# Optimization experiments

Measured on AMD Instinct MI355X. Metric: run time of the kernel, lower is better.

Reference implementation:

```python
import jax, jax.numpy as jnp
import numpy as np

B, N, F_IN = 4, 2048, 256
K, D = 4, 64
NEG_SLOPE = 0.2


def setup_inputs() -> dict:
    key = jax.random.key(0)
    k1, k2, k3, k4, k5 = jax.random.split(key, 5)
    x = jax.random.normal(k1, (B, N, F_IN), dtype=jnp.float32)
    adj = jax.random.randint(k2, (B, N, N), 0, 2, dtype=jnp.int32)
    # xavier_uniform-style params
    def xavier(k, shape):
        fan_in, fan_out = shape[-2], shape[-1]
        lim = np.sqrt(6.0 / (fan_in + fan_out))
        return jax.random.uniform(k, shape, jnp.float32, -lim, lim)
    W = xavier(k3, (K, F_IN, D))
    a_src = xavier(k4, (K, D, 1))
    a_dst = xavier(k5, (K, D, 1))
    return {"x": x, "adj": adj, "W": W, "a_src": a_src, "a_dst": a_dst}


def reference(x, adj, W, a_src, a_dst):
    # Wh: (B, K, N, D)
    Wh = jnp.einsum('bnf,kfd->bknd', x, W)
    e_src = jnp.einsum('bknd,kdo->bkno', Wh, a_src)  # (B,K,N,1)
    e_dst = jnp.einsum('bknd,kdo->bkno', Wh, a_dst)  # (B,K,N,1)
    e = e_src + jnp.swapaxes(e_dst, -2, -1)          # (B,K,N,N)
    e = jnp.where(e > 0, e, NEG_SLOPE * e)           # LeakyReLU(0.2)
    # adjacency mask with forced self-loops (adj + I > 0)
    eye = jnp.eye(e.shape[-1], dtype=bool)
    mask = (adj[:, None, :, :] > 0) | eye            # (B,1|K,N,N)
    e = jnp.where(mask, e, -jnp.inf)
    # numerically-stable softmax matching F_module_softmax
    x_max = jnp.max(e, axis=-1, keepdims=True)
    x_max = jnp.where(jnp.isinf(x_max), 0.0, x_max)
    exp_e = jnp.exp(e - x_max)
    exp_e = jnp.where(jnp.isinf(e), 0.0, exp_e)
    alpha = exp_e / (jnp.sum(exp_e, axis=-1, keepdims=True) + 1e-10)
    # dropout is identity in eval mode
    out = jnp.matmul(alpha, Wh)                      # (B,K,N,D)
    # concat heads: (B,N,K*D)
    Bn, Kn, Nn, Dn = out.shape
    return jnp.transpose(out, (0, 2, 1, 3)).reshape(Bn, Nn, Kn * Dn)
```

## Files before the change

### kernel.cpp

```cpp
#include <hip/hip_runtime.h>

#define NB 4
#define NN 2048
#define NF 256
#define NK 4
#define ND 64
#define NEG 0.2f
#define LOG2E 1.4426950408889634f

typedef _Float16 f16;
typedef _Float16 f16x2 __attribute__((ext_vector_type(2)));
typedef _Float16 f16x4 __attribute__((ext_vector_type(4)));
typedef _Float16 f16x8 __attribute__((ext_vector_type(8)));
typedef float f32x4 __attribute__((ext_vector_type(4)));
typedef float f32x16 __attribute__((ext_vector_type(16)));
typedef unsigned int u32;
typedef unsigned short u16;

__global__ __launch_bounds__(256) void k01(
    const float* __restrict__ x,
    const int*   __restrict__ adj,
    const float* __restrict__ Wm,
    const float* __restrict__ a_src,
    const float* __restrict__ a_dst,
    unsigned int* __restrict__ abit,
    f16* __restrict__ wht,
    float* __restrict__ sbuf,
    f16* __restrict__ ebuf,
    f16* __restrict__ fbuf)
{
    __shared__ f16 wt[64 * 256];

    const int bx  = blockIdx.x;
    const int tid = threadIdx.x;

    if (bx >= 256) {
        const int row = (bx - 256) * 4 + (tid >> 6);
        const int l   = tid & 63;
        const int i   = row & (NN - 1);
        const int* __restrict__ ar = adj + (size_t)row * NN;

        int v[32];
#pragma unroll
        for (int c = 0; c < 32; ++c) v[c] = ar[c * 64 + l];

        unsigned int kx = 0, ky = 0;
#pragma unroll
        for (int c = 0; c < 32; ++c) {
            unsigned long long m = __ballot(v[c] > 0);
            if (l == c) { kx = (unsigned int)m; ky = (unsigned int)(m >> 32); }
        }
        if (l == (i >> 6)) {
            unsigned int sb = 1u << (i & 31);
            if (((i >> 5) & 1) == 0) kx |= sb; else ky |= sb;
        }
        if (l < 32) {
            uint2 kk; kk.x = kx; kk.y = ky;
            *(uint2*)&abit[(size_t)row * 64 + l * 2] = kk;
        }
        return;
    }

    const int gx  = bx & 15;
    const int k   = (bx >> 4) & 3;
    const int b   = bx >> 6;
    const int wv  = tid >> 6;
    const int l   = tid & 63;
    const int q   = l >> 4;
    const int r16 = l & 15;

    for (int fc = 0; fc < 64; ++fc) {
        int f = fc * 4 + wv;
        int d = l;
        wt[d * 256 + (f ^ ((d & 7) << 3))] = (f16)Wm[(k * NF + f) * ND + d];
    }
    __syncthreads();

    const int ncol0 = gx * 128 + wv * 32;
    f32x4 acc[2][4];
#pragma unroll
    for (int nt = 0; nt < 2; ++nt)
#pragma unroll
        for (int dt = 0; dt < 4; ++dt)
            acc[nt][dt] = (f32x4){0.f, 0.f, 0.f, 0.f};

    for (int fs = 0; fs < 16; ++fs) {
        const int f0 = fs * 16 + q * 4;
        f16x4 af[4];
#pragma unroll
        for (int dt = 0; dt < 4; ++dt) {
            int d = dt * 16 + r16;
            af[dt] = *(const f16x4*)&wt[d * 256 + (f0 ^ ((d & 7) << 3))];
        }
#pragma unroll
        for (int nt = 0; nt < 2; ++nt) {
            int n = ncol0 + nt * 16 + r16;
            float4 xv = *(const float4*)&x[((size_t)(b * NN + n)) * NF + f0];
            f16x4 bf = {(f16)xv.x, (f16)xv.y, (f16)xv.z, (f16)xv.w};
#pragma unroll
            for (int dt = 0; dt < 4; ++dt)
                acc[nt][dt] = __builtin_amdgcn_mfma_f32_16x16x16f16(
                    af[dt], bf, acc[nt][dt], 0, 0, 0);
        }
    }

    float asv[4][4], adv[4][4];
#pragma unroll
    for (int dt = 0; dt < 4; ++dt)
#pragma unroll
        for (int rr = 0; rr < 4; ++rr) {
            int d = dt * 16 + q * 4 + rr;
            asv[dt][rr] = a_src[k * ND + d];
            adv[dt][rr] = a_dst[k * ND + d];
        }

    const size_t obase = (size_t)(b * NK + k) * 131072;

#pragma unroll
    for (int nt = 0; nt < 2; ++nt) {
        int n  = ncol0 + nt * 16 + r16;
        const size_t sb_ = obase + (size_t)(n >> 3) * 512 + (n & 7);
        float sp = 0.f, tp = 0.f;
#pragma unroll
        for (int dt = 0; dt < 4; ++dt)
#pragma unroll
            for (int rr = 0; rr < 4; ++rr) {
                float v = acc[nt][dt][rr];
                int d = dt * 16 + q * 4 + rr;
                wht[sb_ + d * 8] = (f16)v;
                sp += v * asv[dt][rr];
                tp += v * adv[dt][rr];
            }
        sp += __shfl_xor(sp, 16);
        sp += __shfl_xor(sp, 32);
        tp += __shfl_xor(tp, 16);
        tp += __shfl_xor(tp, 32);
        if (q == 0) {
            int idx = (b * NK + k) * NN + n;
            sbuf[idx] = sp;
            ebuf[idx] = (f16)__builtin_exp2f(tp * LOG2E);
            fbuf[idx] = (f16)__builtin_exp2f(0.2f * LOG2E * tp);
        }
    }
}

__global__ __launch_bounds__(512) void k2_attn(
    const unsigned int* __restrict__ abit,
    const f16* __restrict__ wht,
    const float* __restrict__ sbuf,
    const f16* __restrict__ ebuf,
    const f16* __restrict__ fbuf,
    float* __restrict__ out)
{
    const int bid = blockIdx.x;
    const int bkv = (bid & 7) | (((bid >> 3) & 1) << 3);
    const int rg  = bid >> 4;
    const int b   = bkv >> 2, k = bkv & 3;
    const int i0  = rg * 64;
    const int tid = threadIdx.x;
    const int w   = tid >> 6;
    const int l   = tid & 63;
    const int r32 = l & 31;
    const int hi  = l >> 5;
    const int row_a = i0 + r32;
    const int row_b = i0 + 32 + r32;

    __shared__ __attribute__((aligned(16))) char pool[75776];
    u16*   el      = (u16*)(pool + 65536);
    u16*   fl      = (u16*)(pool + 69632);
    float* ddenbuf = (float*)(pool + 73728);

    {
        const u16* eb = (const u16*)(ebuf + bkv * NN);
        const u16* fb = (const u16*)(fbuf + bkv * NN);
        *(uint2*)&el[tid * 4] = *(const uint2*)&eb[tid * 4];
        *(uint2*)&fl[tid * 4] = *(const uint2*)&fb[tid * 4];
    }

    const float s_a = sbuf[bkv * NN + row_a];
    const float s_b = sbuf[bkv * NN + row_b];
    const f16 Afa = (f16)__builtin_exp2f(0.8f * LOG2E * fminf(s_a, 0.f));
    const f16 Bfa = (f16)__builtin_exp2f(-0.8f * LOG2E * fmaxf(s_a, 0.f));
    const f16 Afb = (f16)__builtin_exp2f(0.8f * LOG2E * fminf(s_b, 0.f));
    const f16 Bfb = (f16)__builtin_exp2f(-0.8f * LOG2E * fmaxf(s_b, 0.f));
    const f16x2 Af2a = {Afa, Afa}, Bf2a = {Bfa, Bfa};
    const f16x2 Af2b = {Afb, Afb}, Bf2b = {Bfb, Bfb};
    const f16x2 one2 = {(f16)1.0f, (f16)1.0f};

    const unsigned int* __restrict__ abrow_a =
        abit + (size_t)(b * NN + row_a) * 64 + w * 8;
    const unsigned int* __restrict__ abrow_b = abrow_a + 32 * 64;
    uint2 abx_a[4], abx_b[4];
#pragma unroll
    for (int it = 0; it < 4; ++it) {
        abx_a[it] = *(const uint2*)(abrow_a + it * 2);
        abx_b[it] = *(const uint2*)(abrow_b + it * 2);
    }

    const f16* __restrict__ lanep =
        wht + (size_t)bkv * 131072 + (size_t)(w * 32 + hi) * 512 + r32 * 8;

    float den_a = 0.f, den_b = 0.f;
    f32x16 acc[4];
#pragma unroll
    for (int t = 0; t < 4; ++t)
#pragma unroll
        for (int z = 0; z < 16; ++z) acc[t][z] = 0.f;

    __syncthreads();

#define PABUILD(PA, DEN, AF2, BF2, WORD)                                       \
    do {                                                                       \
        const u32 bbyte = ((WORD) >> (((jts & 1) << 4) + (hi << 3))) & 0xffu;  \
        const u32 u = (bbyte << 15) | bbyte;                                   \
        u32 pa_u[4];                                                           \
        _Pragma("unroll") for (int p = 0; p < 4; ++p) {                        \
            f16x2 e2 = __builtin_bit_cast(f16x2, ((const u32*)&E4)[p]);        \
            f16x2 f2 = __builtin_bit_cast(f16x2, ((const u32*)&F4)[p]);        \
            f16x2 w2 = __builtin_elementwise_max((AF2) * e2, (BF2) * f2);      \
            u32 xx = (u >> (2 * p)) & 0x00010001u;                             \
            u32 mm = (xx << 16) - xx;                                          \
            pa_u[p] = __builtin_bit_cast(u32, w2) & mm;                        \
            DEN = __builtin_amdgcn_fdot2(                                      \
                __builtin_bit_cast(f16x2, pa_u[p]), one2, DEN, false);         \
        }                                                                      \
        uint4 pav = {pa_u[0], pa_u[1], pa_u[2], pa_u[3]};                      \
        PA = __builtin_bit_cast(f16x8, pav);                                   \
    } while (0)

#define FRAG_ADDR(st) (lanep + (size_t)(((st) >> 2) * 8 + ((st) & 3) * 2) * 512)
#define JB(st) (w * 256 + ((st) >> 2) * 64 + ((st) & 3) * 16 + hi * 8)

    f16x8 vf[3][2];
    uint4 EF[2][2];
    vf[0][0] = *(const f16x8*)(FRAG_ADDR(0));
    vf[0][1] = *(const f16x8*)(FRAG_ADDR(0) + 256);
    vf[1][0] = *(const f16x8*)(FRAG_ADDR(1));
    vf[1][1] = *(const f16x8*)(FRAG_ADDR(1) + 256);
    EF[0][0] = *(const uint4*)&el[JB(0)];
    EF[0][1] = *(const uint4*)&fl[JB(0)];

#pragma unroll
    for (int st = 0; st < 16; ++st) {
        const int it = st >> 2, jts = st & 3;
        if (st < 14) {
            vf[(st + 2) % 3][0] = *(const f16x8*)(FRAG_ADDR(st + 2));
            vf[(st + 2) % 3][1] = *(const f16x8*)(FRAG_ADDR(st + 2) + 256);
        }
        if (st < 15) {
            EF[(st + 1) & 1][0] = *(const uint4*)&el[JB(st + 1)];
            EF[(st + 1) & 1][1] = *(const uint4*)&fl[JB(st + 1)];
        }
        const uint4 E4 = EF[st & 1][0];
        const uint4 F4 = EF[st & 1][1];
        const u32 word_a = (jts & 2) ? abx_a[it].y : abx_a[it].x;
        const u32 word_b = (jts & 2) ? abx_b[it].y : abx_b[it].x;
        f16x8 pa_a, pa_b;
        PABUILD(pa_a, den_a, Af2a, Bf2a, word_a);
        PABUILD(pa_b, den_b, Af2b, Bf2b, word_b);

        const f16x8 v80 = vf[st % 3][0];
        const f16x8 v81 = vf[st % 3][1];
        acc[0] = __builtin_amdgcn_mfma_f32_32x32x16_f16(pa_a, v80, acc[0], 0, 0, 0);
        acc[1] = __builtin_amdgcn_mfma_f32_32x32x16_f16(pa_a, v81, acc[1], 0, 0, 0);
        acc[2] = __builtin_amdgcn_mfma_f32_32x32x16_f16(pa_b, v80, acc[2], 0, 0, 0);
        acc[3] = __builtin_amdgcn_mfma_f32_32x32x16_f16(pa_b, v81, acc[3], 0, 0, 0);
    }
#undef PABUILD
#undef FRAG_ADDR
#undef JB

    den_a += __shfl_xor(den_a, 32);
    den_b += __shfl_xor(den_b, 32);
    if (hi == 0) {
        ddenbuf[w * 64 + r32]      = den_a;
        ddenbuf[w * 64 + 32 + r32] = den_b;
    }

#define TDUMP(reg)                                                             \
    do {                                                                       \
        float* rb = (float*)(pool + (reg) * 16384) + l * 64;                   \
        _Pragma("unroll") for (int t = 0; t < 4; ++t)                          \
        _Pragma("unroll") for (int sub = 0; sub < 4; ++sub) {                  \
            f32x4 vv = {acc[t][sub * 4], acc[t][sub * 4 + 1],                  \
                        acc[t][sub * 4 + 2], acc[t][sub * 4 + 3]};             \
            *(f32x4*)&rb[((t * 4 + sub) ^ (l & 15)) << 2] = vv;                \
        }                                                                      \
    } while (0)
#define TADD(reg)                                                              \
    do {                                                                       \
        const float* rb = (const float*)(pool + (reg) * 16384) + l * 64;       \
        _Pragma("unroll") for (int t = 0; t < 4; ++t)                          \
        _Pragma("unroll") for (int sub = 0; sub < 4; ++sub) {                  \
            f32x4 vv = *(const f32x4*)&rb[((t * 4 + sub) ^ (l & 15)) << 2];    \
            _Pragma("unroll") for (int m = 0; m < 4; ++m)                      \
                acc[t][sub * 4 + m] += vv[m];                                  \
        }                                                                      \
    } while (0)

    __syncthreads();
    if (w >= 4) TDUMP(w - 4);
    __syncthreads();
    if (w < 4) TADD(w);
    if (w == 2 || w == 3) TDUMP(w);
    __syncthreads();
    if (w < 2) TADD(w + 2);
    if (w == 1) TDUMP(1);
    __syncthreads();
    if (w == 0) {
        TADD(1);
        float* dsum = (float*)(pool + 16384);
        float dd = 0.f;
#pragma unroll
        for (int ww = 0; ww < 8; ++ww) dd += ddenbuf[ww * 64 + l];
        dsum[l] = 1.f / (dd + 1e-10f);
        float* op = out + ((size_t)(b * NN) + i0) * (NK * ND) + k * ND;
#pragma unroll
        for (int t = 0; t < 4; ++t)
#pragma unroll
            for (int rr = 0; rr < 16; ++rr) {
                const int row = (t >> 1) * 32 + (rr & 3) + 8 * (rr >> 2) + 4 * hi;
                op[(size_t)row * (NK * ND) + (t & 1) * 32 + r32] =
                    acc[t][rr] * dsum[row];
            }
    }
#undef TDUMP
#undef TADD
}

extern "C" void kernel_launch(void* const* d_in, const int* in_sizes, int n_in,
                              void* d_out, int out_size, void* d_ws, size_t ws_size,
                              hipStream_t stream) {
    const float* x     = (const float*)d_in[0];
    const int*   adj   = (const int*)d_in[1];
    const float* Wm    = (const float*)d_in[2];
    const float* a_src = (const float*)d_in[3];
    const float* a_dst = (const float*)d_in[4];
    float* out = (float*)d_out;

    char* ws = (char*)d_ws;
    f16*   wht  = (f16*)ws;
    float* sbuf = (float*)(ws + (4u << 20));
    f16*   ebuf = (f16*)(ws + (4u << 20) + (128u << 10));
    f16*   fbuf = (f16*)(ws + (4u << 20) + (192u << 10));
    unsigned int* abit = (unsigned int*)(ws + (4u << 20) + (256u << 10));

    k01<<<dim3(256 + NB * NN / 4), 256, 0, stream>>>(
        x, adj, Wm, a_src, a_dst, abit, wht, sbuf, ebuf, fbuf);
    k2_attn<<<dim3(512), 512, 0, stream>>>(
        abit, wht, sbuf, ebuf, fbuf, out);
}
```

Baseline: 41.13 us.

## Vectorize W staging, stage Wh stores through LDS, compute softmax denominators via MFMA

The projection kernel now loads W with float4 reads instead of scalar loads. It also writes the Wh tile through an LDS transpose so global stores become 16-byte f16x8 writes rather than scattered 2-byte stores. In the attention kernel, the per-lane fdot2 denominator accumulation is replaced by two extra MFMAs against an all-ones operand, which moves VALU work onto the matrix units. The trade-off is extra syncs and LDS traffic in the first kernel, plus 50% more MFMA issue and extra accumulator registers in the second.

Measured after the change: 44.64 us. 8.5% more time.

```diff
diff --git a/kernel.cpp b/kernel.cpp
--- a/kernel.cpp
+++ b/kernel.cpp
@@ -69,10 +69,15 @@
     const int q   = l >> 4;
     const int r16 = l & 15;
 
-    for (int fc = 0; fc < 64; ++fc) {
-        int f = fc * 4 + wv;
-        int d = l;
-        wt[d * 256 + (f ^ ((d & 7) << 3))] = (f16)Wm[(k * NF + f) * ND + d];
+#pragma unroll
+    for (int p = 0; p < 16; ++p) {
+        const int f  = p * 16 + (tid >> 4);
+        const int d0 = (tid & 15) * 4;
+        float4 wv4 = *(const float4*)&Wm[(size_t)(k * NF + f) * ND + d0];
+        wt[(d0 + 0) * 256 + (f ^ (((d0 + 0) & 7) << 3))] = (f16)wv4.x;
+        wt[(d0 + 1) * 256 + (f ^ (((d0 + 1) & 7) << 3))] = (f16)wv4.y;
+        wt[(d0 + 2) * 256 + (f ^ (((d0 + 2) & 7) << 3))] = (f16)wv4.z;
+        wt[(d0 + 3) * 256 + (f ^ (((d0 + 3) & 7) << 3))] = (f16)wv4.w;
     }
     __syncthreads();
 
@@ -114,22 +119,16 @@
             adv[dt][rr] = a_dst[k * ND + d];
         }
 
-    const size_t obase = (size_t)(b * NK + k) * 131072;
-
 #pragma unroll
     for (int nt = 0; nt < 2; ++nt) {
-        int n  = ncol0 + nt * 16 + r16;
-        const size_t sb_ = obase + (size_t)(n >> 3) * 512 + (n & 7);
+        int n = ncol0 + nt * 16 + r16;
         float sp = 0.f, tp = 0.f;
 #pragma unroll
         for (int dt = 0; dt < 4; ++dt)
 #pragma unroll
             for (int rr = 0; rr < 4; ++rr) {
-                float v = acc[nt][dt][rr];
-                int d = dt * 16 + q * 4 + rr;
-                wht[sb_ + d * 8] = (f16)v;
-                sp += v * asv[dt][rr];
-                tp += v * adv[dt][rr];
+                sp += acc[nt][dt][rr] * asv[dt][rr];
+                tp += acc[nt][dt][rr] * adv[dt][rr];
             }
         sp += __shfl_xor(sp, 16);
         sp += __shfl_xor(sp, 32);
@@ -140,6 +139,31 @@
             sbuf[idx] = sp;
             ebuf[idx] = (f16)__builtin_exp2f(tp * LOG2E);
             fbuf[idx] = (f16)__builtin_exp2f(0.2f * LOG2E * tp);
+        }
+    }
+
+    __syncthreads();
+    f16* lt = wt;
+#pragma unroll
+    for (int nt = 0; nt < 2; ++nt) {
+        const int nl = wv * 32 + nt * 16 + r16;
+#pragma unroll
+        for (int dt = 0; dt < 4; ++dt)
+#pragma unroll
+            for (int rr = 0; rr < 4; ++rr) {
+                int d = dt * 16 + q * 4 + rr;
+                lt[d * 136 + nl] = (f16)acc[nt][dt][rr];
+            }
+    }
+    __syncthreads();
+    {
+        const size_t obase = (size_t)(b * NK + k) * 131072 + (size_t)gx * 8192;
+        const int o  = tid >> 4;
+        const int d0 = (tid & 15) * 4;
+#pragma unroll
+        for (int z = 0; z < 4; ++z) {
+            f16x8 v8 = *(const f16x8*)&lt[(d0 + z) * 136 + o * 8];
+            *(f16x8*)&wht[obase + (size_t)o * 512 + (d0 + z) * 8] = v8;
         }
     }
 }
@@ -185,7 +209,8 @@
     const f16 Bfb = (f16)__builtin_exp2f(-0.8f * LOG2E * fmaxf(s_b, 0.f));
     const f16x2 Af2a = {Afa, Afa}, Bf2a = {Bfa, Bfa};
     const f16x2 Af2b = {Afb, Afb}, Bf2b = {Bfb, Bfb};
-    const f16x2 one2 = {(f16)1.0f, (f16)1.0f};
+    const f16 h1 = (f16)1.0f;
+    const f16x8 ones8 = {h1, h1, h1, h1, h1, h1, h1, h1};
 
     const unsigned int* __restrict__ abrow_a =
         abit + (size_t)(b * NN + row_a) * 64 + w * 8;
@@ -200,16 +225,19 @@
     const f16* __restrict__ lanep =
         wht + (size_t)bkv * 131072 + (size_t)(w * 32 + hi) * 512 + r32 * 8;
 
-    float den_a = 0.f, den_b = 0.f;
-    f32x16 acc[4];
+    f32x16 acc[4], accd[2];
 #pragma unroll
     for (int t = 0; t < 4; ++t)
 #pragma unroll
         for (int z = 0; z < 16; ++z) acc[t][z] = 0.f;
-
-    __syncthreads();
-
-#define PABUILD(PA, DEN, AF2, BF2, WORD)                                       \
+#pragma unroll
+    for (int t = 0; t < 2; ++t)
+#pragma unroll
+        for (int z = 0; z < 16; ++z) accd[t][z] = 0.f;
+
+    __syncthreads();
+
+#define PABUILD(PA, AF2, BF2, WORD)                                            \
     do {                                                                       \
         const u32 bbyte = ((WORD) >> (((jts & 1) << 4) + (hi << 3))) & 0xffu;  \
         const u32 u = (bbyte << 15) | bbyte;                                   \
@@ -221,8 +249,6 @@
             u32 xx = (u >> (2 * p)) & 0x00010001u;                             \
             u32 mm = (xx << 16) - xx;                                          \
             pa_u[p] = __builtin_bit_cast(u32, w2) & mm;                        \
-            DEN = __builtin_amdgcn_fdot2(                                      \
-                __builtin_bit_cast(f16x2, pa_u[p]), one2, DEN, false);         \
         }                                                                      \
         uint4 pav = {pa_u[0], pa_u[1], pa_u[2], pa_u[3]};                      \
         PA = __builtin_bit_cast(f16x8, pav);                                   \
@@ -256,8 +282,8 @@
         const u32 word_a = (jts & 2) ? abx_a[it].y : abx_a[it].x;
         const u32 word_b = (jts & 2) ? abx_b[it].y : abx_b[it].x;
         f16x8 pa_a, pa_b;
-        PABUILD(pa_a, den_a, Af2a, Bf2a, word_a);
-        PABUILD(pa_b, den_b, Af2b, Bf2b, word_b);
+        PABUILD(pa_a, Af2a, Bf2a, word_a);
+        PABUILD(pa_b, Af2b, Bf2b, word_b);
 
         const f16x8 v80 = vf[st % 3][0];
         const f16x8 v81 = vf[st % 3][1];
@@ -265,16 +291,20 @@
         acc[1] = __builtin_amdgcn_mfma_f32_32x32x16_f16(pa_a, v81, acc[1], 0, 0, 0);
         acc[2] = __builtin_amdgcn_mfma_f32_32x32x16_f16(pa_b, v80, acc[2], 0, 0, 0);
         acc[3] = __builtin_amdgcn_mfma_f32_32x32x16_f16(pa_b, v81, acc[3], 0, 0, 0);
+        accd[0] = __builtin_amdgcn_mfma_f32_32x32x16_f16(pa_a, ones8, accd[0], 0, 0, 0);
+        accd[1] = __builtin_amdgcn_mfma_f32_32x32x16_f16(pa_b, ones8, accd[1], 0, 0, 0);
     }
 #undef PABUILD
 #undef FRAG_ADDR
 #undef JB
 
-    den_a += __shfl_xor(den_a, 32);
-    den_b += __shfl_xor(den_b, 32);
-    if (hi == 0) {
-        ddenbuf[w * 64 + r32]      = den_a;
-        ddenbuf[w * 64 + 32 + r32] = den_b;
+    if (r32 == 0) {
+#pragma unroll
+        for (int rr = 0; rr < 16; ++rr) {
+            const int row = (rr & 3) + 8 * (rr >> 2) + 4 * hi;
+            ddenbuf[w * 64 + row]      = accd[0][rr];
+            ddenbuf[w * 64 + 32 + row] = accd[1][rr];
+        }
     }
 
 #define TDUMP(reg)                                                             \
```
